# Optimization experiments

Hardware: AMD Instinct MI355X
Metric: run time of the kernel (lower is better)

## Reference

```python
import jax, jax.numpy as jnp
import numpy as np
from jax import lax

B, M, D, N = 256, 1024, 128, 26  # batch, seq_len, feat_dim, num_labels


def setup_inputs() -> dict:
    key = jax.random.key(0)
    k1, k2, k3, k4 = jax.random.split(key, 4)
    X = jax.random.normal(k1, (B, M, D), dtype=jnp.float32)
    labels = jax.random.randint(k2, (B, M), 0, N, dtype=jnp.int32)
    # Learned CRF params (zeros in the module; random here for a non-degenerate test).
    W = jax.random.normal(k3, (N, D), dtype=jnp.float32) * 0.05
    T = jax.random.normal(k4, (N, N), dtype=jnp.float32) * 0.1
    return {"X": X, "labels": labels, "W": W, "T": T}


def _seq_log_prob(x, y, W, T):
    # x: [M, D], y: [M] int labels.
    # Original forward_messages (prob space): f[i,a] = exp(x_i.W_a) * sum_b exp(T[b,a]) f[i-1,b]
    # Computed here equivalently in log space for numerical stability.
    e = x @ W.T  # [M, N] emission scores x_i . W_a

    def step(lf, e_i):
        # logsumexp over previous label b of (lf[b] + T[b, a])
        lf_new = e_i + jax.nn.logsumexp(lf[:, None] + T, axis=0)
        return lf_new, None

    lf_last, _ = lax.scan(step, e[0], e[1:])
    logZ = jax.nn.logsumexp(lf_last)
    unnorm = jnp.sum(jnp.take_along_axis(e, y[:, None], axis=1)) \
        + jnp.sum(T[y[:-1], y[1:]])
    return unnorm - logZ


def reference(X, labels, W, T):
    # CRF.forward with identity conv stack: mean log p(y | x) over the batch.
    log_probs = jax.vmap(lambda x, y: _seq_log_prob(x, y, W, T))(X, labels)
    return jnp.mean(log_probs)
```

## Files before the change

kernel.cpp:

```cpp
#include <hip/hip_runtime.h>

#define CB 256
#define CM 1024
#define CD 128
#define CN 26

__device__ inline float rfl_f(float x) {
    return __int_as_float(__builtin_amdgcn_readfirstlane(__float_as_int(x)));
}
__device__ inline float rdl_f(float x, int lane) {
#if __has_builtin(__builtin_amdgcn_readlane)
    return __int_as_float(__builtin_amdgcn_readlane(__float_as_int(x), lane));
#else
    return __shfl(x, lane, 64);
#endif
}
__device__ inline float fexp2(float x) {
#if __has_builtin(__builtin_amdgcn_exp2f)
    return __builtin_amdgcn_exp2f(x);
#else
    return exp2f(x);
#endif
}
__device__ inline float flog2(float x) {
#if __has_builtin(__builtin_amdgcn_logf)
    return __builtin_amdgcn_logf(x);
#else
    return log2f(x);
#endif
}

__global__ __launch_bounds__(256, 1) void emit_kernel(
    const float* __restrict__ X, const float* __restrict__ W,
    const int* __restrict__ labels, const float* __restrict__ T,
    float* __restrict__ E, float* __restrict__ out) {
    __shared__ float Ws[CN * CD];
    __shared__ float rsum[4];

    const int t = threadIdx.x;
    const int row0 = blockIdx.x * 1024 + t * 4;

    for (int i = t; i < CN * CD; i += 256) Ws[i] = W[i];
    __syncthreads();

    float acc[4][CN];
#pragma unroll
    for (int g = 0; g < 4; ++g)
#pragma unroll
        for (int a = 0; a < CN; ++a) acc[g][a] = 0.f;

    const float4* __restrict__ x40 =
        reinterpret_cast<const float4*>(X + (size_t)row0 * CD);
    const float4* Ws4 = reinterpret_cast<const float4*>(Ws);

#pragma unroll 1
    for (int c = 0; c < 16; ++c) {
        float4 xv[4][2];
#pragma unroll
        for (int g = 0; g < 4; ++g) {
            xv[g][0] = x40[g * 32 + c * 2];
            xv[g][1] = x40[g * 32 + c * 2 + 1];
        }
#pragma unroll
        for (int a = 0; a < CN; ++a) {
            float4 w0 = Ws4[a * 32 + c * 2];
            float4 w1 = Ws4[a * 32 + c * 2 + 1];
#pragma unroll
            for (int g = 0; g < 4; ++g) {
                float s = acc[g][a];
                s = fmaf(xv[g][0].x, w0.x, s);
                s = fmaf(xv[g][0].y, w0.y, s);
                s = fmaf(xv[g][0].z, w0.z, s);
                s = fmaf(xv[g][0].w, w0.w, s);
                s = fmaf(xv[g][1].x, w1.x, s);
                s = fmaf(xv[g][1].y, w1.y, s);
                s = fmaf(xv[g][1].z, w1.z, s);
                s = fmaf(xv[g][1].w, w1.w, s);
                acc[g][a] = s;
            }
        }
    }

    const float LOG2E = 1.4426950408889634f;
#pragma unroll
    for (int g = 0; g < 4; ++g) {
        float2* e2 =
            reinterpret_cast<float2*>(E + (size_t)(row0 + g) * CN);
#pragma unroll
        for (int a = 0; a < CN / 2; ++a)
            e2[a] = make_float2(acc[g][2 * a] * LOG2E,
                                acc[g][2 * a + 1] * LOG2E);
    }

    float us = 0.f;
#pragma unroll
    for (int g = 0; g < 4; ++g) {
        int row = row0 + g;
        int y = labels[row];
        float sel = acc[g][0];
#pragma unroll
        for (int a = 1; a < CN; ++a) sel = (y == a) ? acc[g][a] : sel;
        us += sel;
        if (row & (CM - 1)) {
            int yp = labels[row - 1];
            us += T[yp * CN + y];
        }
    }
#pragma unroll
    for (int off = 32; off > 0; off >>= 1) us += __shfl_xor(us, off, 64);
    if ((t & 63) == 0) rsum[t >> 6] = us;
    __syncthreads();
    if (t == 0)
        atomicAdd(out, (rsum[0] + rsum[1] + rsum[2] + rsum[3]) * (1.f / CB));
}

template <bool BWD>
__device__ void run_half(float* __restrict__ base, const float* __restrict__ T,
                         int a, int l) {
    float AT[CN];
#pragma unroll
    for (int k = 0; k < CN; ++k)
        AT[k] = expf(BWD ? T[a * CN + k] : T[k * CN + a]);

    const int S = BWD ? -CN : CN;
    const float* __restrict__ Eb = base + (BWD ? (size_t)1023 * CN : 0) + a;

    float f, L = 0.f;
    float epf[8];
    const float* pf;
    if (BWD) {
        f = 1.f;
#pragma unroll
        for (int k = 0; k < 8; ++k) epf[k] = Eb[k * S];
        pf = Eb + 8 * S;
    } else {
        f = fexp2(Eb[0]);
#pragma unroll
        for (int k = 0; k < 8; ++k) epf[k] = Eb[(1 + k) * S];
        pf = Eb + 9 * S;
    }

    auto step = [&](float e_cur, bool renorm) {
        float p = fexp2(e_cur);
        float x = BWD ? p * f : f;
        float d0 = 0.f, d1 = 0.f, d2 = 0.f, d3 = 0.f;
#pragma unroll
        for (int b = 0; b < 24; b += 4) {
            d0 = fmaf(AT[b + 0], rdl_f(x, b + 0), d0);
            d1 = fmaf(AT[b + 1], rdl_f(x, b + 1), d1);
            d2 = fmaf(AT[b + 2], rdl_f(x, b + 2), d2);
            d3 = fmaf(AT[b + 3], rdl_f(x, b + 3), d3);
        }
        d0 = fmaf(AT[24], rdl_f(x, 24), d0);
        d1 = fmaf(AT[25], rdl_f(x, 25), d1);
        float d = (d0 + d1) + (d2 + d3);
        f = BWD ? d : p * d;
        if (renorm) {
            float fr = rfl_f(f);
            int k2 = (int)((__float_as_uint(fr) >> 23) & 255) - 127;
            f = ldexpf(f, -k2);
            L += (float)k2;
        }
    };

    const int NMAIN = BWD ? 63 : 62;
    for (int it = 0; it < NMAIN; ++it) {
#pragma unroll
        for (int k = 0; k < 8; ++k) {
            float e_cur = epf[k];
            epf[k] = pf[k * S];
            step(e_cur, k == 7);
        }
        pf += 8 * S;
    }
    if (BWD) {
#pragma unroll
        for (int k = 0; k < 8; ++k) step(epf[k], k == 7);
    } else {
#pragma unroll
        for (int k = 0; k < 8; ++k) {
            float e_cur = epf[k];
            if (k < 7) epf[k] = pf[k * S];
            step(e_cur, k == 7);
        }
#pragma unroll
        for (int k = 0; k < 7; ++k) step(epf[k], false);
    }

    {
        float fr = rfl_f(f);
        int k2 = (int)((__float_as_uint(fr) >> 23) & 255) - 127;
        f = ldexpf(f, -k2);
        L += (float)k2;
    }

    base[(BWD ? (size_t)1023 * CN : 0) + a] = f;
    if (l == 0) base[(BWD ? (size_t)1022 * CN : (size_t)CN)] = L;
}

__global__ __launch_bounds__(64) void crf_half_kernel(
    float* __restrict__ E, const float* __restrict__ T) {
    const int s = blockIdx.x >> 1;
    const int l = threadIdx.x;
    const int a = (l < CN) ? l : (CN - 1);
    float* base = E + (size_t)s * CM * CN;
    if (blockIdx.x & 1)
        run_half<true>(base, T, a, l);
    else
        run_half<false>(base, T, a, l);
}

__global__ __launch_bounds__(64) void crf_combine_kernel(
    const float* __restrict__ E, float* __restrict__ out) {
    const int s = blockIdx.x;
    const int l = threadIdx.x;
    const float LN2 = 0.6931471805599453f;
    const float* base = E + (size_t)s * CM * CN;

    float v = 0.f;
    if (l < CN) v = base[l] * base[(size_t)1023 * CN + l];
#pragma unroll
    for (int off = 32; off > 0; off >>= 1) v += __shfl_xor(v, off, 64);

    if (l == 0) {
        float Lf = base[CN];
        float Lb = base[(size_t)1022 * CN];
        float logZ = LN2 * (Lf + Lb + flog2(v));
        atomicAdd(out, -logZ * (1.f / (float)CB));
    }
}

extern "C" void kernel_launch(void* const* d_in, const int* in_sizes, int n_in,
                              void* d_out, int out_size, void* d_ws,
                              size_t ws_size, hipStream_t stream) {
    const float* X = (const float*)d_in[0];
    const int* labels = (const int*)d_in[1];
    const float* W = (const float*)d_in[2];
    const float* T = (const float*)d_in[3];
    float* out = (float*)d_out;
    float* E = (float*)d_ws;

    hipMemsetAsync(d_out, 0, sizeof(float), stream);
    emit_kernel<<<(CB * CM) / 1024, 256, 0, stream>>>(X, W, labels, T, E, out);
    crf_half_kernel<<<CB * 2, 64, 0, stream>>>(E, T);
    crf_combine_kernel<<<CB, 64, 0, stream>>>(E, out);
}
```

Measured before the change: 283.0 us.

## Halve rows per thread in emission GEMM and double-buffer X loads

Each thread in the emission kernel now computes 2 rows instead of 4, which doubles the grid to 512 blocks. Launch bounds are raised to allow 2 blocks per CU, cutting accumulator register pressure and raising occupancy. The chunk loop is unrolled by two with ping-pong register buffers, so the next chunk of X is prefetched while the current one is multiplied. In exchange, each LDS W read is reused across fewer rows, and more blocks reload W and issue atomics.

New measurement: 384.8 us. 36.0% more time.

```diff
diff --git a/kernel.cpp b/kernel.cpp
--- a/kernel.cpp
+++ b/kernel.cpp
@@ -30,7 +30,7 @@
 #endif
 }
 
-__global__ __launch_bounds__(256, 1) void emit_kernel(
+__global__ __launch_bounds__(256, 2) void emit_kernel(
     const float* __restrict__ X, const float* __restrict__ W,
     const int* __restrict__ labels, const float* __restrict__ T,
     float* __restrict__ E, float* __restrict__ out) {
@@ -38,14 +38,14 @@
     __shared__ float rsum[4];
 
     const int t = threadIdx.x;
-    const int row0 = blockIdx.x * 1024 + t * 4;
+    const int row0 = blockIdx.x * 512 + t * 2;
 
     for (int i = t; i < CN * CD; i += 256) Ws[i] = W[i];
     __syncthreads();
 
-    float acc[4][CN];
-#pragma unroll
-    for (int g = 0; g < 4; ++g)
+    float acc[2][CN];
+#pragma unroll
+    for (int g = 0; g < 2; ++g)
 #pragma unroll
         for (int a = 0; a < CN; ++a) acc[g][a] = 0.f;
 
@@ -53,37 +53,68 @@
         reinterpret_cast<const float4*>(X + (size_t)row0 * CD);
     const float4* Ws4 = reinterpret_cast<const float4*>(Ws);
 
+    float4 xa[2][2], xb[2][2];
+#pragma unroll
+    for (int g = 0; g < 2; ++g) {
+        xa[g][0] = x40[g * 32 + 0];
+        xa[g][1] = x40[g * 32 + 1];
+    }
+
 #pragma unroll 1
-    for (int c = 0; c < 16; ++c) {
-        float4 xv[4][2];
-#pragma unroll
-        for (int g = 0; g < 4; ++g) {
-            xv[g][0] = x40[g * 32 + c * 2];
-            xv[g][1] = x40[g * 32 + c * 2 + 1];
+    for (int c = 0; c < 16; c += 2) {
+#pragma unroll
+        for (int g = 0; g < 2; ++g) {
+            xb[g][0] = x40[g * 32 + (c + 1) * 2];
+            xb[g][1] = x40[g * 32 + (c + 1) * 2 + 1];
         }
 #pragma unroll
         for (int a = 0; a < CN; ++a) {
             float4 w0 = Ws4[a * 32 + c * 2];
             float4 w1 = Ws4[a * 32 + c * 2 + 1];
 #pragma unroll
-            for (int g = 0; g < 4; ++g) {
+            for (int g = 0; g < 2; ++g) {
                 float s = acc[g][a];
-                s = fmaf(xv[g][0].x, w0.x, s);
-                s = fmaf(xv[g][0].y, w0.y, s);
-                s = fmaf(xv[g][0].z, w0.z, s);
-                s = fmaf(xv[g][0].w, w0.w, s);
-                s = fmaf(xv[g][1].x, w1.x, s);
-                s = fmaf(xv[g][1].y, w1.y, s);
-                s = fmaf(xv[g][1].z, w1.z, s);
-                s = fmaf(xv[g][1].w, w1.w, s);
+                s = fmaf(xa[g][0].x, w0.x, s);
+                s = fmaf(xa[g][0].y, w0.y, s);
+                s = fmaf(xa[g][0].z, w0.z, s);
+                s = fmaf(xa[g][0].w, w0.w, s);
+                s = fmaf(xa[g][1].x, w1.x, s);
+                s = fmaf(xa[g][1].y, w1.y, s);
+                s = fmaf(xa[g][1].z, w1.z, s);
+                s = fmaf(xa[g][1].w, w1.w, s);
                 acc[g][a] = s;
             }
         }
+        if (c + 2 < 16) {
+#pragma unroll
+            for (int g = 0; g < 2; ++g) {
+                xa[g][0] = x40[g * 32 + (c + 2) * 2];
+                xa[g][1] = x40[g * 32 + (c + 2) * 2 + 1];
+            }
+        }
+#pragma unroll
+        for (int a = 0; a < CN; ++a) {
+            float4 w0 = Ws4[a * 32 + (c + 1) * 2];
+            float4 w1 = Ws4[a * 32 + (c + 1) * 2 + 1];
+#pragma unroll
+            for (int g = 0; g < 2; ++g) {
+                float s = acc[g][a];
+                s = fmaf(xb[g][0].x, w0.x, s);
+                s = fmaf(xb[g][0].y, w0.y, s);
+                s = fmaf(xb[g][0].z, w0.z, s);
+                s = fmaf(xb[g][0].w, w0.w, s);
+                s = fmaf(xb[g][1].x, w1.x, s);
+                s = fmaf(xb[g][1].y, w1.y, s);
+                s = fmaf(xb[g][1].z, w1.z, s);
+                s = fmaf(xb[g][1].w, w1.w, s);
+                acc[g][a] = s;
+            }
+        }
     }
 
     const float LOG2E = 1.4426950408889634f;
 #pragma unroll
-    for (int g = 0; g < 4; ++g) {
+    for (int g = 0; g < 2; ++g) {
         float2* e2 =
             reinterpret_cast<float2*>(E + (size_t)(row0 + g) * CN);
 #pragma unroll
@@ -94,7 +125,7 @@
 
     float us = 0.f;
 #pragma unroll
-    for (int g = 0; g < 4; ++g) {
+    for (int g = 0; g < 2; ++g) {
         int row = row0 + g;
         int y = labels[row];
         float sel = acc[g][0];
@@ -241,7 +272,7 @@
     float* E = (float*)d_ws;
 
     hipMemsetAsync(d_out, 0, sizeof(float), stream);
-    emit_kernel<<<(CB * CM) / 1024, 256, 0, stream>>>(X, W, labels, T, E, out);
+    emit_kernel<<<(CB * CM) / 512, 256, 0, stream>>>(X, W, labels, T, E, out);
     crf_half_kernel<<<CB * 2, 64, 0, stream>>>(E, T);
     crf_combine_kernel<<<CB, 64, 0, stream>>>(E, out);
 }
```
